# Kernel optimization log

Hardware: AMD Instinct MI355X
Metric: run time of the kernel (lower is better)

Reference implementation:

```python
import jax, jax.numpy as jnp
import numpy as np

B, C, IMG, P = 8, 6, 384, 16
DIM, HEADS, DEPTH, MLP, NCLS = 768, 12, 4, 3072, 1000
N = (IMG // P) ** 2            # 576 patches
DH = DIM // HEADS              # 64
PATCH_DIM = C * P * P          # 1536


def setup_inputs() -> dict:
    key = jax.random.key(0)
    ks = jax.random.split(key, 13)
    f = lambda k, shp, s=0.02: jax.random.normal(k, shp, jnp.float32) * s
    return {
        "x": jax.random.normal(ks[0], (B, C, IMG, IMG), jnp.float32),
        "patch_w": f(ks[1], (PATCH_DIM, DIM)),
        "patch_b": f(ks[2], (DIM,)),
        "ln1_g": jnp.ones((DEPTH, DIM), jnp.float32),
        "ln1_b": jnp.zeros((DEPTH, DIM), jnp.float32),
        "w_qkv": f(ks[3], (DEPTH, DIM, 3 * DIM)),
        "bias_att": f(ks[4], (DEPTH, HEADS, N, N), 0.5),
        "w_out": f(ks[5], (DEPTH, DIM, DIM)),
        "ln2_g": jnp.ones((DEPTH, DIM), jnp.float32),
        "ln2_b": jnp.zeros((DEPTH, DIM), jnp.float32),
        "w1": f(ks[6], (DEPTH, DIM, MLP)),
        "b1": f(ks[7], (DEPTH, MLP)),
        "w2": f(ks[8], (DEPTH, MLP, DIM)),
        "b2": f(ks[9], (DEPTH, DIM)),
        "lnh_g": jnp.ones((DIM,), jnp.float32),
        "lnh_b": jnp.zeros((DIM,), jnp.float32),
        "w_head": f(ks[10], (DIM, NCLS)),
        "b_head": f(ks[11], (NCLS,)),
    }


def _ln(x, g, b, eps=1e-5):
    m = x.mean(-1, keepdims=True)
    v = ((x - m) ** 2).mean(-1, keepdims=True)
    return (x - m) * jax.lax.rsqrt(v + eps) * g + b


def _patchify(x, patch_w, patch_b):
    # Rearrange 'b c (h p1) (w p2) -> b (h w) (p1 p2 c)' then Linear(patch_dim, dim)
    b = x.shape[0]
    g = IMG // P
    x = x.reshape(b, C, g, P, g, P).transpose(0, 2, 4, 3, 5, 1).reshape(b, g * g, PATCH_DIM)
    return x @ patch_w + patch_b


def _forward(x, patch_w, patch_b, ln1_g, ln1_b, w_qkv, bias_att, w_out,
             ln2_g, ln2_b, w1, b1, w2, b2, lnh_g, lnh_b, w_head, b_head):
    scale = DH ** -0.5
    tok = _patchify(x, patch_w, patch_b)  # [B, N, DIM]; pos_info='mul_att_normed' -> no pos_embed added

    def block(t, p):
        l1g, l1b, wqkv, bias, wout, l2g, l2b, ww1, bb1, ww2, bb2 = p
        h = _ln(t, l1g, l1b)
        qkv = h @ wqkv                                     # [B, N, 3*DIM]
        q, k, v = jnp.split(qkv, 3, axis=-1)
        rs = lambda a: a.reshape(t.shape[0], N, HEADS, DH).transpose(0, 2, 1, 3)
        q, k, v = rs(q), rs(k), rs(v)                      # [B, H, N, DH]
        dots = jnp.einsum('bhid,bhjd->bhij', q, k) * scale
        # mul_att_normed: softmax(qk) * softmax(bias), renormalized over keys
        attn = jax.nn.softmax(dots, axis=-1) * jax.nn.softmax(bias, axis=-1)[None]
        attn = attn / attn.sum(-1, keepdims=True)
        o = jnp.einsum('bhij,bhjd->bhid', attn, v)
        o = o.transpose(0, 2, 1, 3).reshape(t.shape[0], N, DIM) @ wout
        t = t + o
        h2 = _ln(t, l2g, l2b)
        t = t + (jax.nn.gelu(h2 @ ww1 + bb1, approximate=False) @ ww2 + bb2)
        return t, None

    tok, _ = jax.lax.scan(block, tok,
                          (ln1_g, ln1_b, w_qkv, bias_att, w_out,
                           ln2_g, ln2_b, w1, b1, w2, b2))
    pooled = tok.mean(axis=1)                              # mean-pool tokens
    return _ln(pooled, lnh_g, lnh_b) @ w_head + b_head     # [B, NCLS]


def reference(x, patch_w, patch_b, ln1_g, ln1_b, w_qkv, bias_att, w_out,
              ln2_g, ln2_b, w1, b1, w2, b2, lnh_g, lnh_b, w_head, b_head):
    return _forward(x, patch_w, patch_b, ln1_g, ln1_b, w_qkv, bias_att, w_out,
                    ln2_g, ln2_b, w1, b1, w2, b2, lnh_g, lnh_b, w_head, b_head)
```

## Files before the change

### kernel.cpp

```cpp
#include <hip/hip_runtime.h>
#include <hip/hip_bf16.h>

typedef __attribute__((ext_vector_type(8))) short bf16x8;
typedef __attribute__((ext_vector_type(4))) float f32x4;

#define DEVI __device__ __forceinline__

DEVI unsigned short f2bf_bits(float f) {
    __hip_bfloat16 h = __float2bfloat16(f);
    return *reinterpret_cast<unsigned short*>(&h);
}

DEVI void gload_lds16(const void* g, void* lds) {
    __builtin_amdgcn_global_load_lds(
        (const __attribute__((address_space(1))) unsigned int*)g,
        (__attribute__((address_space(3))) unsigned int*)lds, 16, 0, 0);
}

template <int N> DEVI void wait_vm() {
    if constexpr (N == 0) asm volatile("s_waitcnt vmcnt(0)" ::: "memory");
    else if constexpr (N == 3) asm volatile("s_waitcnt vmcnt(3)" ::: "memory");
    else if constexpr (N == 6) asm volatile("s_waitcnt vmcnt(6)" ::: "memory");
    else if constexpr (N == 12) asm volatile("s_waitcnt vmcnt(12)" ::: "memory");
    __builtin_amdgcn_sched_barrier(0);
}

DEVI int2 remap2d(int bid, int total, int gx) {
    int q = total >> 3, r = total & 7, x = bid & 7, l = bid >> 3;
    int seq = (x < r ? x * (q + 1) : r * (q + 1) + (x - r) * q) + l;
    int g4 = seq / (4 * gx);
    int rem = seq - g4 * 4 * gx;
    return {g4 * 4 + (rem & 3), rem >> 2};
}

__global__ __launch_bounds__(256) void patchify_kernel(const float* __restrict__ x,
                                                       unsigned short* __restrict__ patches)
{
    size_t t8 = (size_t)blockIdx.x * 256 + threadIdx.x;
    int jq = (int)(t8 % 48);
    size_t t = t8 / 48;
    int r = (int)(t % 384); t /= 384;
    int c = (int)(t % 6);
    int b = (int)(t / 6);
    int j = jq * 8;
    int gh = r >> 4, p1 = r & 15, gw = j >> 4, p2 = j & 15;
    int prow = b * 576 + gh * 24 + gw;
    int pcol = c * 256 + p1 * 16 + p2;
    const float* src = x + ((((size_t)b * 6 + c) * 384 + r) * 384 + j);
    float4 v0 = ((const float4*)src)[0];
    float4 v1 = ((const float4*)src)[1];
    ushort u[8] = { f2bf_bits(v0.x), f2bf_bits(v0.y), f2bf_bits(v0.z), f2bf_bits(v0.w),
                    f2bf_bits(v1.x), f2bf_bits(v1.y), f2bf_bits(v1.z), f2bf_bits(v1.w) };
    *(int4*)&patches[(size_t)prow * 1536 + pcol] = *(int4*)u;
}

__global__ __launch_bounds__(256) void convT_patch_kernel(const float* __restrict__ W,
                                                          __hip_bfloat16* __restrict__ Wt)
{
    __shared__ float tile[32][33];
    int n0 = blockIdx.x * 32, kp0 = blockIdx.y * 32;
    int tx = threadIdx.x & 31, ty = threadIdx.x >> 5;
#pragma unroll
    for (int i = 0; i < 4; i++) {
        int kp = kp0 + ty + 8 * i;
        int k = (kp & 255) * 6 + (kp >> 8);
        tile[ty + 8 * i][tx] = W[(size_t)k * 768 + n0 + tx];
    }
    __syncthreads();
#pragma unroll
    for (int i = 0; i < 4; i++)
        Wt[(size_t)(n0 + ty + 8 * i) * 1536 + kp0 + tx] = __float2bfloat16(tile[tx][ty + 8 * i]);
}

DEVI void convT_body(const float* __restrict__ W, __hip_bfloat16* __restrict__ Wt,
                     int K, int N, int k0, int n0, int tid)
{
    __shared__ float tile[32][33];
    int tx = tid & 31, ty = tid >> 5;
#pragma unroll
    for (int i = 0; i < 4; i++)
        tile[ty + 8 * i][tx] = W[(size_t)(k0 + ty + 8 * i) * N + n0 + tx];
    __syncthreads();
#pragma unroll
    for (int i = 0; i < 4; i++)
        Wt[(size_t)(n0 + ty + 8 * i) * K + k0 + tx] = __float2bfloat16(tile[tx][ty + 8 * i]);
}

__global__ __launch_bounds__(256) void convT4_kernel(const float* __restrict__ wqkv,
                                                     const float* __restrict__ wout,
                                                     const float* __restrict__ w1,
                                                     const float* __restrict__ w2,
                                                     __hip_bfloat16* __restrict__ dst)
{
    int bt = blockIdx.x;
    const float* W; __hip_bfloat16* Wt; int K, N, lt;
    if (bt < 1728)      { W = wqkv; K = 768;  N = 2304; lt = bt;        Wt = dst; }
    else if (bt < 2304) { W = wout; K = 768;  N = 768;  lt = bt - 1728; Wt = dst + 1769472; }
    else if (bt < 4608) { W = w1;   K = 768;  N = 3072; lt = bt - 2304; Wt = dst + 2359296; }
    else                { W = w2;   K = 3072; N = 768;  lt = bt - 4608; Wt = dst + 4718592; }
    int tn = N >> 5;
    convT_body(W, Wt, K, N, (lt / tn) * 32, (lt % tn) * 32, threadIdx.x);
}

DEVI void st_ln(float* p, float v) { *p = v; }
DEVI void st_ln(__hip_bfloat16* p, float v) { *p = __float2bfloat16(v); }

template <typename OutT>
__global__ __launch_bounds__(256) void ln_kernel(const float* __restrict__ x,
                                                 const float* __restrict__ g,
                                                 const float* __restrict__ b,
                                                 OutT* __restrict__ out)
{
    int row = blockIdx.x, tid = threadIdx.x;
    const float* xr = x + (size_t)row * 768;
    float v0 = xr[tid], v1 = xr[tid + 256], v2 = xr[tid + 512];
    float s = v0 + v1 + v2;
    float s2 = v0 * v0 + v1 * v1 + v2 * v2;
#pragma unroll
    for (int m = 32; m >= 1; m >>= 1) { s += __shfl_xor(s, m); s2 += __shfl_xor(s2, m); }
    __shared__ float red[8];
    int w = tid >> 6;
    if ((tid & 63) == 0) { red[w] = s; red[4 + w] = s2; }
    __syncthreads();
    s = red[0] + red[1] + red[2] + red[3];
    s2 = red[4] + red[5] + red[6] + red[7];
    float mean = s * (1.0f / 768.0f);
    float var = s2 * (1.0f / 768.0f) - mean * mean;
    float rstd = rsqrtf(var + 1e-5f);
    OutT* orow = out + (size_t)row * 768;
    st_ln(&orow[tid], (v0 - mean) * rstd * g[tid] + b[tid]);
    st_ln(&orow[tid + 256], (v1 - mean) * rstd * g[tid + 256] + b[tid + 256]);
    st_ln(&orow[tid + 512], (v2 - mean) * rstd * g[tid + 512] + b[tid + 512]);
}

template <bool BIAS, bool RESID, bool GELU>
__global__ __launch_bounds__(256, 3) void gemm_bt_kernel(
    const __hip_bfloat16* __restrict__ A,
    const __hip_bfloat16* __restrict__ Bt,
    const float* __restrict__ bias,
    const float* __restrict__ resid,
    float* __restrict__ Cf,
    int M, int N, int K, int gx)
{
    constexpr int BM = 64, SL = 3;
    __shared__ __align__(16) __hip_bfloat16 As[3][BM * 32];
    __shared__ __align__(16) __hip_bfloat16 Bs[3][128 * 32];
    const int tid = threadIdx.x;
    const int wid = tid >> 6, lane = tid & 63;
    const int g = lane >> 4, l16 = lane & 15;
    const int wm = (wid >> 1) * 32, wn = (wid & 1) * 64;

    int2 bc = remap2d(blockIdx.x, gridDim.x, gx);
    const int bm = bc.x * BM, bn = bc.y * 128;

    const int sr = tid >> 2;
    const int csrc = (lane & 3) ^ ((lane >> 3) & 3);
    const int sdst = sr * 32 + (lane & 3) * 8;
    size_t aOff = (size_t)(bm + sr) * K + csrc * 8;
    size_t bOff[2];
#pragma unroll
    for (int i = 0; i < 2; i++) bOff[i] = (size_t)(bn + i * 64 + sr) * K + csrc * 8;

    auto stage = [&](__hip_bfloat16* asb, __hip_bfloat16* bsb, int tq) {
        const __hip_bfloat16* ap = A + tq * 32;
        const __hip_bfloat16* bp = Bt + tq * 32;
        gload_lds16(ap + aOff, asb + sdst);
#pragma unroll
        for (int i = 0; i < 2; i++) gload_lds16(bp + bOff[i], bsb + i * 2048 + sdst);
    };

    const int pSw = (l16 >> 1) & 3;
    f32x4 acc[2][4] = {};
    const int nt = K >> 5;

    stage(As[0], Bs[0], 0);
    stage(As[1], Bs[1], 1);
    stage(As[2], Bs[2], 2);
    wait_vm<2 * SL>();
    __builtin_amdgcn_s_barrier();
    __builtin_amdgcn_sched_barrier(0);

    for (int t = 0; t < nt; t += 3) {
#pragma unroll
        for (int u = 0; u < 3; u++) {
            const int tc = t + u;
            bf16x8 af[2], bfr[4];
#pragma unroll
            for (int mi = 0; mi < 2; mi++)
                af[mi] = *(const bf16x8*)&As[u][(wm + mi * 16 + l16) * 32 + ((g ^ pSw) << 3)];
#pragma unroll
            for (int ni = 0; ni < 4; ni++)
                bfr[ni] = *(const bf16x8*)&Bs[u][(wn + ni * 16 + l16) * 32 + ((g ^ pSw) << 3)];
            __builtin_amdgcn_s_setprio(1);
#pragma unroll
            for (int mi = 0; mi < 2; mi++)
#pragma unroll
                for (int ni = 0; ni < 4; ni++)
                    acc[mi][ni] = __builtin_amdgcn_mfma_f32_16x16x32_bf16(af[mi], bfr[ni], acc[mi][ni], 0, 0, 0);
            __builtin_amdgcn_s_setprio(0);

            asm volatile("s_waitcnt lgkmcnt(0)" ::: "memory");
            __builtin_amdgcn_sched_barrier(0);
            __builtin_amdgcn_s_barrier();
            __builtin_amdgcn_sched_barrier(0);

            if (tc + 3 < nt) stage(As[u], Bs[u], tc + 3);
            if (tc + 1 < nt) {
                if (tc + 4 <= nt)      wait_vm<2 * SL>();
                else if (tc + 3 == nt) wait_vm<SL>();
                else                   wait_vm<0>();
                __builtin_amdgcn_s_barrier();
                __builtin_amdgcn_sched_barrier(0);
            }
        }
    }

#pragma unroll
    for (int mi = 0; mi < 2; mi++) {
#pragma unroll
        for (int ni = 0; ni < 4; ni++) {
            int gcol = bn + wn + ni * 16 + l16;
            float bval = 0.0f;
            if (BIAS) bval = bias[gcol];
#pragma unroll
            for (int r = 0; r < 4; r++) {
                int grow = bm + wm + mi * 16 + 4 * g + r;
                float v = acc[mi][ni][r] + bval;
                if (GELU) v = 0.5f * v * (1.0f + erff(v * 0.70710678118654752f));
                if (RESID) v += resid[(size_t)grow * N + gcol];
                Cf[(size_t)grow * N + gcol] = v;
            }
        }
    }
}

template <bool BIAS, bool GELU>
__global__ __launch_bounds__(256, 2) void gemm_wide_kernel(
    const __hip_bfloat16* __restrict__ A,
    const __hip_bfloat16* __restrict__ Bt,
    const float* __restrict__ bias,
    __hip_bfloat16* __restrict__ Cb,
    int M, int N, int K, int gx)
{
    constexpr int SL = 6;
    __shared__ __align__(16) __hip_bfloat16 As[3][128 * 32];
    __shared__ __align__(16) __hip_bfloat16 Bs[3][256 * 32];
    const int tid = threadIdx.x;
    const int wid = tid >> 6, lane = tid & 63;
    const int g = lane >> 4, l16 = lane & 15;
    const int wm = (wid >> 1) * 64, wn = (wid & 1) * 128;

    int2 bc = remap2d(blockIdx.x, gridDim.x, gx);
    const int bm = bc.x * 128, bn = bc.y * 256;

    const int sr = tid >> 2;
    const int csrc = (lane & 3) ^ ((lane >> 3) & 3);
    const int sdst = sr * 32 + (lane & 3) * 8;
    size_t aOff[2], bOff[4];
#pragma unroll
    for (int i = 0; i < 2; i++) aOff[i] = (size_t)(bm + i * 64 + sr) * K + csrc * 8;
#pragma unroll
    for (int i = 0; i < 4; i++) bOff[i] = (size_t)(bn + i * 64 + sr) * K + csrc * 8;

    auto stage = [&](__hip_bfloat16* asb, __hip_bfloat16* bsb, int tq) {
        const __hip_bfloat16* ap = A + tq * 32;
        const __hip_bfloat16* bp = Bt + tq * 32;
#pragma unroll
        for (int i = 0; i < 2; i++) gload_lds16(ap + aOff[i], asb + i * 2048 + sdst);
#pragma unroll
        for (int i = 0; i < 4; i++) gload_lds16(bp + bOff[i], bsb + i * 2048 + sdst);
    };

    const int pSw = (l16 >> 1) & 3;
    f32x4 acc[4][8] = {};
    const int nt = K >> 5;

    stage(As[0], Bs[0], 0);
    stage(As[1], Bs[1], 1);
    stage(As[2], Bs[2], 2);
    wait_vm<2 * SL>();
    __builtin_amdgcn_s_barrier();
    __builtin_amdgcn_sched_barrier(0);

    for (int t = 0; t < nt; t += 3) {
#pragma unroll
        for (int u = 0; u < 3; u++) {
            const int tc = t + u;
            bf16x8 af[4], bfr[8];
#pragma unroll
            for (int mi = 0; mi < 4; mi++)
                af[mi] = *(const bf16x8*)&As[u][(wm + mi * 16 + l16) * 32 + ((g ^ pSw) << 3)];
#pragma unroll
            for (int ni = 0; ni < 8; ni++)
                bfr[ni] = *(const bf16x8*)&Bs[u][(wn + ni * 16 + l16) * 32 + ((g ^ pSw) << 3)];
            __builtin_amdgcn_s_setprio(1);
#pragma unroll
            for (int mi = 0; mi < 4; mi++)
#pragma unroll
                for (int ni = 0; ni < 8; ni++)
                    acc[mi][ni] = __builtin_amdgcn_mfma_f32_16x16x32_bf16(af[mi], bfr[ni], acc[mi][ni], 0, 0, 0);
            __builtin_amdgcn_s_setprio(0);

            asm volatile("s_waitcnt lgkmcnt(0)" ::: "memory");
            __builtin_amdgcn_sched_barrier(0);
            __builtin_amdgcn_s_barrier();
            __builtin_amdgcn_sched_barrier(0);

            if (tc + 3 < nt) stage(As[u], Bs[u], tc + 3);
            if (tc + 1 < nt) {
                if (tc + 4 <= nt)      wait_vm<2 * SL>();
                else if (tc + 3 == nt) wait_vm<SL>();
                else                   wait_vm<0>();
                __builtin_amdgcn_s_barrier();
                __builtin_amdgcn_sched_barrier(0);
            }
        }
    }

    __hip_bfloat16* scr = &As[0][0] + wid * (16 * 136);
#pragma unroll
    for (int mi = 0; mi < 4; mi++) {
#pragma unroll
        for (int ni = 0; ni < 8; ni++) {
            int gcol = bn + wn + ni * 16 + l16;
            float bval = 0.0f;
            if (BIAS) bval = bias[gcol];
#pragma unroll
            for (int r = 0; r < 4; r++) {
                float v = acc[mi][ni][r] + bval;
                if (GELU) v = 0.5f * v * (1.0f + erff(v * 0.70710678118654752f));
                scr[(4 * g + r) * 136 + ni * 16 + l16] = __float2bfloat16(v);
            }
        }
        asm volatile("s_waitcnt lgkmcnt(0)" ::: "memory");
        __builtin_amdgcn_sched_barrier(0);
#pragma unroll
        for (int q2 = 0; q2 < 4; q2++) {
            int idx = q2 * 64 + lane;
            int row16 = idx >> 4, ch = idx & 15;
            bf16x8 vv = *(const bf16x8*)&scr[row16 * 136 + ch * 8];
            int grow = bm + wm + mi * 16 + row16;
            *(int4*)&Cb[(size_t)grow * N + bn + wn + ch * 8] = *(int4*)&vv;
        }
        asm volatile("s_waitcnt lgkmcnt(0)" ::: "memory");
        __builtin_amdgcn_sched_barrier(0);
    }
}

__global__ __launch_bounds__(256) void attn_kernel(const __hip_bfloat16* __restrict__ qkvb,
                                                   const float* __restrict__ bias,
                                                   unsigned short* __restrict__ o)
{
    const int seq = (blockIdx.x & 7) * 108 + (blockIdx.x >> 3);
    const int bb = seq & 7, qt = (seq >> 3) % 9, h = seq / 72;
    const int q0 = qt * 64;
    const int tid = threadIdx.x;
    const int wq = tid >> 6, lane = tid & 63, g = lane >> 4, l16 = lane & 15;

    __shared__ __align__(16) unsigned short Qs[64 * 72];
    __shared__ __align__(16) unsigned short Ks[64 * 72];
    __shared__ __align__(16) unsigned short Vt[64 * 72];
    __shared__ __align__(16) unsigned short Ps[4][16 * 72];

    {
        int r = tid >> 2, cb = (tid & 3) * 16;
        const int4* s4 = (const int4*)&qkvb[(size_t)(bb * 576 + q0 + r) * 2304 + h * 64 + cb];
        int4* d4 = (int4*)&Qs[r * 72 + cb];
        d4[0] = s4[0]; d4[1] = s4[1];
    }
    __syncthreads();
    bf16x8 qf0 = *(const bf16x8*)&Qs[(wq * 16 + l16) * 72 + g * 8];
    bf16x8 qf1 = *(const bf16x8*)&Qs[(wq * 16 + l16) * 72 + 32 + g * 8];

    float m_r[4] = {-1e30f, -1e30f, -1e30f, -1e30f};
    float l_r[4] = {0.f, 0.f, 0.f, 0.f};
    f32x4 oa[4] = {};
    const float* bias_h = bias + (size_t)h * 576 * 576;
    const float scale = 0.125f;

    for (int kt = 0; kt < 576; kt += 64) {
        {
            int r = tid >> 2, cb = (tid & 3) * 16;
            const int4* s4 = (const int4*)&qkvb[(size_t)(bb * 576 + kt + r) * 2304 + 768 + h * 64 + cb];
            int4* d4 = (int4*)&Ks[r * 72 + cb];
            d4[0] = s4[0]; d4[1] = s4[1];
            int key = tid & 63, d0 = (tid >> 6) * 16;
            const unsigned short* vs = (const unsigned short*)&qkvb[(size_t)(bb * 576 + kt + key) * 2304 + 1536 + h * 64 + d0];
            bf16x8 v0 = *(const bf16x8*)vs;
            bf16x8 v1 = *(const bf16x8*)(vs + 8);
#pragma unroll
            for (int e = 0; e < 8; e++) {
                Vt[(d0 + e) * 72 + key] = (unsigned short)v0[e];
                Vt[(d0 + 8 + e) * 72 + key] = (unsigned short)v1[e];
            }
        }
        __syncthreads();

        float bl[4][4];
#pragma unroll
        for (int kc = 0; kc < 4; kc++)
#pragma unroll
            for (int r = 0; r < 4; r++) {
                int q = q0 + wq * 16 + 4 * g + r;
                bl[kc][r] = bias_h[(size_t)q * 576 + kt + kc * 16 + l16];
            }

        f32x4 sc[4] = {};
        __builtin_amdgcn_s_setprio(1);
#pragma unroll
        for (int kc = 0; kc < 4; kc++) {
            bf16x8 kf0 = *(const bf16x8*)&Ks[(kc * 16 + l16) * 72 + g * 8];
            bf16x8 kf1 = *(const bf16x8*)&Ks[(kc * 16 + l16) * 72 + 32 + g * 8];
            sc[kc] = __builtin_amdgcn_mfma_f32_16x16x32_bf16(qf0, kf0, sc[kc], 0, 0, 0);
            sc[kc] = __builtin_amdgcn_mfma_f32_16x16x32_bf16(qf1, kf1, sc[kc], 0, 0, 0);
        }
        __builtin_amdgcn_s_setprio(0);

        float sv[4][4], mt[4] = {-1e30f, -1e30f, -1e30f, -1e30f};
#pragma unroll
        for (int kc = 0; kc < 4; kc++)
#pragma unroll
            for (int r = 0; r < 4; r++) {
                float s = sc[kc][r] * scale + bl[kc][r];
                sv[kc][r] = s;
                mt[r] = fmaxf(mt[r], s);
            }
#pragma unroll
        for (int r = 0; r < 4; r++)
#pragma unroll
            for (int m = 1; m < 16; m <<= 1) mt[r] = fmaxf(mt[r], __shfl_xor(mt[r], m));

        float sf[4];
#pragma unroll
        for (int r = 0; r < 4; r++) {
            float mn = fmaxf(m_r[r], mt[r]);
            sf[r] = __expf(m_r[r] - mn);
            m_r[r] = mn;
        }
        float rs[4] = {0.f, 0.f, 0.f, 0.f};
#pragma unroll
        for (int kc = 0; kc < 4; kc++)
#pragma unroll
            for (int r = 0; r < 4; r++) {
                float p = __expf(sv[kc][r] - m_r[r]);
                rs[r] += p;
                Ps[wq][(4 * g + r) * 72 + kc * 16 + l16] = f2bf_bits(p);
            }
#pragma unroll
        for (int r = 0; r < 4; r++) {
#pragma unroll
            for (int m = 1; m < 16; m <<= 1) rs[r] += __shfl_xor(rs[r], m);
            l_r[r] = l_r[r] * sf[r] + rs[r];
        }
#pragma unroll
        for (int dt = 0; dt < 4; dt++)
#pragma unroll
            for (int r = 0; r < 4; r++) oa[dt][r] *= sf[r];

        asm volatile("s_waitcnt lgkmcnt(0)" ::: "memory");

        __builtin_amdgcn_s_setprio(1);
#pragma unroll
        for (int s = 0; s < 2; s++) {
            bf16x8 pf = *(const bf16x8*)&Ps[wq][l16 * 72 + s * 32 + g * 8];
#pragma unroll
            for (int dt = 0; dt < 4; dt++) {
                bf16x8 vf = *(const bf16x8*)&Vt[(dt * 16 + l16) * 72 + s * 32 + g * 8];
                oa[dt] = __builtin_amdgcn_mfma_f32_16x16x32_bf16(pf, vf, oa[dt], 0, 0, 0);
            }
        }
        __builtin_amdgcn_s_setprio(0);
        __syncthreads();
    }

#pragma unroll
    for (int dt = 0; dt < 4; dt++)
#pragma unroll
        for (int r = 0; r < 4; r++) {
            int q = q0 + wq * 16 + 4 * g + r;
            float v = oa[dt][r] / l_r[r];
            o[(size_t)(bb * 576 + q) * 768 + h * 64 + dt * 16 + l16] = f2bf_bits(v);
        }
}

__global__ __launch_bounds__(256) void pool_kernel(const float* __restrict__ tok, float* __restrict__ pooled)
{
    int d = blockIdx.x * 256 + threadIdx.x;
    int b = blockIdx.y;
    float s = 0.0f;
    for (int n = 0; n < 576; n++) s += tok[(size_t)(b * 576 + n) * 768 + d];
    pooled[b * 768 + d] = s * (1.0f / 576.0f);
}

__global__ __launch_bounds__(256) void head_kernel(const float* __restrict__ lnp,
                                                   const float* __restrict__ w,
                                                   const float* __restrict__ bh,
                                                   float* __restrict__ out)
{
    int c = blockIdx.x * 256 + threadIdx.x;
    int b = blockIdx.y;
    if (c >= 1000) return;
    float s = bh[c];
    for (int d = 0; d < 768; d++) s += lnp[b * 768 + d] * w[(size_t)d * 1000 + c];
    out[b * 1000 + c] = s;
}

extern "C" void kernel_launch(void* const* d_in, const int* in_sizes, int n_in,
                              void* d_out, int out_size, void* d_ws, size_t ws_size,
                              hipStream_t stream)
{
    const float* x = (const float*)d_in[0];
    const float* patch_w = (const float*)d_in[1];
    const float* patch_b = (const float*)d_in[2];
    const float* ln1_g = (const float*)d_in[3];
    const float* ln1_b = (const float*)d_in[4];
    const float* w_qkv = (const float*)d_in[5];
    const float* bias_att = (const float*)d_in[6];
    const float* w_out = (const float*)d_in[7];
    const float* ln2_g = (const float*)d_in[8];
    const float* ln2_b = (const float*)d_in[9];
    const float* w1 = (const float*)d_in[10];
    const float* b1 = (const float*)d_in[11];
    const float* w2 = (const float*)d_in[12];
    const float* b2 = (const float*)d_in[13];
    const float* lnh_g = (const float*)d_in[14];
    const float* lnh_b = (const float*)d_in[15];
    const float* w_head = (const float*)d_in[16];
    const float* b_head = (const float*)d_in[17];
    float* out = (float*)d_out;

    char* ws = (char*)d_ws;
    float* tok = (float*)(ws + 0);
    __hip_bfloat16* qkv_bf = (__hip_bfloat16*)(ws + 14155776);
    float* pooled = (float*)(ws + 56623104);
    float* pooledln = (float*)(ws + 56647680);
    __hip_bfloat16* patches = (__hip_bfloat16*)(ws + 56672256);
    __hip_bfloat16* lw = patches;
    __hip_bfloat16* h_bf = (__hip_bfloat16*)(ws + 70828032);
    __hip_bfloat16* o_bf = (__hip_bfloat16*)(ws + 77905920);
    __hip_bfloat16* hid_bf = (__hip_bfloat16*)(ws + 84983808);
    __hip_bfloat16* wbuf = (__hip_bfloat16*)(ws + 113295360);

    patchify_kernel<<<3456, 256, 0, stream>>>(x, (unsigned short*)patches);
    convT_patch_kernel<<<dim3(24, 48), 256, 0, stream>>>(patch_w, wbuf);
    gemm_bt_kernel<true, false, false><<<432, 256, 0, stream>>>(
        patches, wbuf, patch_b, nullptr, tok, 4608, 768, 1536, 6);

    for (int l = 0; l < 4; l++) {
        convT4_kernel<<<6912, 256, 0, stream>>>(
            w_qkv + (size_t)l * 768 * 2304, w_out + (size_t)l * 768 * 768,
            w1 + (size_t)l * 768 * 3072, w2 + (size_t)l * 3072 * 768, lw);
        ln_kernel<__hip_bfloat16><<<4608, 256, 0, stream>>>(tok, ln1_g + l * 768, ln1_b + l * 768, h_bf);
        gemm_wide_kernel<false, false><<<324, 256, 0, stream>>>(
            h_bf, lw, nullptr, qkv_bf, 4608, 2304, 768, 9);
        attn_kernel<<<864, 256, 0, stream>>>(
            qkv_bf, bias_att + (size_t)l * 12 * 576 * 576, (unsigned short*)o_bf);
        gemm_bt_kernel<false, true, false><<<432, 256, 0, stream>>>(
            o_bf, lw + 1769472, nullptr, tok, tok, 4608, 768, 768, 6);
        ln_kernel<__hip_bfloat16><<<4608, 256, 0, stream>>>(tok, ln2_g + l * 768, ln2_b + l * 768, h_bf);
        gemm_wide_kernel<true, true><<<432, 256, 0, stream>>>(
            h_bf, lw + 2359296, b1 + l * 3072, hid_bf, 4608, 3072, 768, 12);
        gemm_bt_kernel<true, true, false><<<432, 256, 0, stream>>>(
            hid_bf, lw + 4718592, b2 + l * 768, tok, tok, 4608, 768, 3072, 6);
    }

    pool_kernel<<<dim3(3, 8), 256, 0, stream>>>(tok, pooled);
    ln_kernel<float><<<8, 256, 0, stream>>>(pooled, lnh_g, lnh_b, pooledln);
    head_kernel<<<dim3(4, 8), 256, 0, stream>>>(pooledln, w_head, b_head, out);
}
```

Measured before the change: 910.3 us.

## Store residual stream in bf16 with LDS-staged vectorized GEMM epilogue

Switches the token/residual buffer from fp32 to bf16, so the LayerNorm, pooling and residual-add GEMMs read and write half the bytes. The narrow GEMM epilogue now stages each warp's tile through shared memory and writes 16-byte vectors, with the residual also loaded as vectors. Block scheduling changes to a simple column-major remap, and the MFMA priority hints are removed. The residual accumulation now rounds to bf16 at every layer, which loses precision.

```diff
diff --git a/kernel.cpp b/kernel.cpp
--- a/kernel.cpp
+++ b/kernel.cpp
@@ -9,6 +9,10 @@
 DEVI unsigned short f2bf_bits(float f) {
     __hip_bfloat16 h = __float2bfloat16(f);
     return *reinterpret_cast<unsigned short*>(&h);
+}
+DEVI float bfbits2f(unsigned short u) {
+    __hip_bfloat16 h = *reinterpret_cast<__hip_bfloat16*>(&u);
+    return __bfloat162float(h);
 }
 
 DEVI void gload_lds16(const void* g, void* lds) {
@@ -25,12 +29,10 @@
     __builtin_amdgcn_sched_barrier(0);
 }
 
-DEVI int2 remap2d(int bid, int total, int gx) {
+DEVI int2 remap_cm(int bid, int total, int nrow) {
     int q = total >> 3, r = total & 7, x = bid & 7, l = bid >> 3;
     int seq = (x < r ? x * (q + 1) : r * (q + 1) + (x - r) * q) + l;
-    int g4 = seq / (4 * gx);
-    int rem = seq - g4 * 4 * gx;
-    return {g4 * 4 + (rem & 3), rem >> 2};
+    return {seq % nrow, seq / nrow};
 }
 
 __global__ __launch_bounds__(256) void patchify_kernel(const float* __restrict__ x,
@@ -102,18 +104,20 @@
     convT_body(W, Wt, K, N, (lt / tn) * 32, (lt % tn) * 32, threadIdx.x);
 }
 
+DEVI float ld_ln(const float* p) { return *p; }
+DEVI float ld_ln(const __hip_bfloat16* p) { return __bfloat162float(*p); }
 DEVI void st_ln(float* p, float v) { *p = v; }
 DEVI void st_ln(__hip_bfloat16* p, float v) { *p = __float2bfloat16(v); }
 
-template <typename OutT>
-__global__ __launch_bounds__(256) void ln_kernel(const float* __restrict__ x,
+template <typename InT, typename OutT>
+__global__ __launch_bounds__(256) void ln_kernel(const InT* __restrict__ x,
                                                  const float* __restrict__ g,
                                                  const float* __restrict__ b,
                                                  OutT* __restrict__ out)
 {
     int row = blockIdx.x, tid = threadIdx.x;
-    const float* xr = x + (size_t)row * 768;
-    float v0 = xr[tid], v1 = xr[tid + 256], v2 = xr[tid + 512];
+    const InT* xr = x + (size_t)row * 768;
+    float v0 = ld_ln(&xr[tid]), v1 = ld_ln(&xr[tid + 256]), v2 = ld_ln(&xr[tid + 512]);
     float s = v0 + v1 + v2;
     float s2 = v0 * v0 + v1 * v1 + v2 * v2;
 #pragma unroll
@@ -133,14 +137,14 @@
     st_ln(&orow[tid + 512], (v2 - mean) * rstd * g[tid + 512] + b[tid + 512]);
 }
 
-template <bool BIAS, bool RESID, bool GELU>
+template <bool BIAS, bool RESID>
 __global__ __launch_bounds__(256, 3) void gemm_bt_kernel(
     const __hip_bfloat16* __restrict__ A,
     const __hip_bfloat16* __restrict__ Bt,
     const float* __restrict__ bias,
-    const float* __restrict__ resid,
-    float* __restrict__ Cf,
-    int M, int N, int K, int gx)
+    const __hip_bfloat16* __restrict__ resid,
+    __hip_bfloat16* __restrict__ Cb,
+    int M, int N, int K, int nrow)
 {
     constexpr int BM = 64, SL = 3;
     __shared__ __align__(16) __hip_bfloat16 As[3][BM * 32];
@@ -150,7 +154,7 @@
     const int g = lane >> 4, l16 = lane & 15;
     const int wm = (wid >> 1) * 32, wn = (wid & 1) * 64;
 
-    int2 bc = remap2d(blockIdx.x, gridDim.x, gx);
+    int2 bc = remap_cm(blockIdx.x, gridDim.x, nrow);
     const int bm = bc.x * BM, bn = bc.y * 128;
 
     const int sr = tid >> 2;
@@ -191,13 +195,11 @@
 #pragma unroll
             for (int ni = 0; ni < 4; ni++)
                 bfr[ni] = *(const bf16x8*)&Bs[u][(wn + ni * 16 + l16) * 32 + ((g ^ pSw) << 3)];
-            __builtin_amdgcn_s_setprio(1);
 #pragma unroll
             for (int mi = 0; mi < 2; mi++)
 #pragma unroll
                 for (int ni = 0; ni < 4; ni++)
                     acc[mi][ni] = __builtin_amdgcn_mfma_f32_16x16x32_bf16(af[mi], bfr[ni], acc[mi][ni], 0, 0, 0);
-            __builtin_amdgcn_s_setprio(0);
 
             asm volatile("s_waitcnt lgkmcnt(0)" ::: "memory");
             __builtin_amdgcn_sched_barrier(0);
@@ -215,22 +217,35 @@
         }
     }
 
+    __hip_bfloat16* scr = &As[0][0] + wid * (16 * 72);
 #pragma unroll
     for (int mi = 0; mi < 2; mi++) {
 #pragma unroll
         for (int ni = 0; ni < 4; ni++) {
-            int gcol = bn + wn + ni * 16 + l16;
             float bval = 0.0f;
-            if (BIAS) bval = bias[gcol];
-#pragma unroll
-            for (int r = 0; r < 4; r++) {
-                int grow = bm + wm + mi * 16 + 4 * g + r;
-                float v = acc[mi][ni][r] + bval;
-                if (GELU) v = 0.5f * v * (1.0f + erff(v * 0.70710678118654752f));
-                if (RESID) v += resid[(size_t)grow * N + gcol];
-                Cf[(size_t)grow * N + gcol] = v;
-            }
-        }
+            if (BIAS) bval = bias[bn + wn + ni * 16 + l16];
+#pragma unroll
+            for (int r = 0; r < 4; r++)
+                scr[(4 * g + r) * 72 + ni * 16 + l16] = __float2bfloat16(acc[mi][ni][r] + bval);
+        }
+        asm volatile("s_waitcnt lgkmcnt(0)" ::: "memory");
+        __builtin_amdgcn_sched_barrier(0);
+#pragma unroll
+        for (int q2 = 0; q2 < 2; q2++) {
+            int row16 = q2 * 8 + (lane >> 3), ch = lane & 7;
+            bf16x8 vv = *(const bf16x8*)&scr[row16 * 72 + ch * 8];
+            int grow = bm + wm + mi * 16 + row16;
+            size_t off = (size_t)grow * N + bn + wn + ch * 8;
+            if (RESID) {
+                bf16x8 rv = *(const bf16x8*)&resid[off];
+#pragma unroll
+                for (int e = 0; e < 8; e++)
+                    vv[e] = (short)f2bf_bits(bfbits2f((unsigned short)vv[e]) + bfbits2f((unsigned short)rv[e]));
+            }
+            *(int4*)&Cb[off] = *(int4*)&vv;
+        }
+        asm volatile("s_waitcnt lgkmcnt(0)" ::: "memory");
+        __builtin_amdgcn_sched_barrier(0);
     }
 }
 
@@ -240,7 +255,7 @@
     const __hip_bfloat16* __restrict__ Bt,
     const float* __restrict__ bias,
     __hip_bfloat16* __restrict__ Cb,
-    int M, int N, int K, int gx)
+    int M, int N, int K, int nrow)
 {
     constexpr int SL = 6;
     __shared__ __align__(16) __hip_bfloat16 As[3][128 * 32];
@@ -250,7 +265,7 @@
     const int g = lane >> 4, l16 = lane & 15;
     const int wm = (wid >> 1) * 64, wn = (wid & 1) * 128;
 
-    int2 bc = remap2d(blockIdx.x, gridDim.x, gx);
+    int2 bc = remap_cm(blockIdx.x, gridDim.x, nrow);
     const int bm = bc.x * 128, bn = bc.y * 256;
 
     const int sr = tid >> 2;
@@ -293,13 +308,11 @@
 #pragma unroll
             for (int ni = 0; ni < 8; ni++)
                 bfr[ni] = *(const bf16x8*)&Bs[u][(wn + ni * 16 + l16) * 32 + ((g ^ pSw) << 3)];
-            __builtin_amdgcn_s_setprio(1);
 #pragma unroll
             for (int mi = 0; mi < 4; mi++)
 #pragma unroll
                 for (int ni = 0; ni < 8; ni++)
                     acc[mi][ni] = __builtin_amdgcn_mfma_f32_16x16x32_bf16(af[mi], bfr[ni], acc[mi][ni], 0, 0, 0);
-            __builtin_amdgcn_s_setprio(0);
 
             asm volatile("s_waitcnt lgkmcnt(0)" ::: "memory");
             __builtin_amdgcn_sched_barrier(0);
@@ -322,9 +335,8 @@
     for (int mi = 0; mi < 4; mi++) {
 #pragma unroll
         for (int ni = 0; ni < 8; ni++) {
-            int gcol = bn + wn + ni * 16 + l16;
             float bval = 0.0f;
-            if (BIAS) bval = bias[gcol];
+            if (BIAS) bval = bias[bn + wn + ni * 16 + l16];
 #pragma unroll
             for (int r = 0; r < 4; r++) {
                 float v = acc[mi][ni][r] + bval;
@@ -483,12 +495,13 @@
         }
 }
 
-__global__ __launch_bounds__(256) void pool_kernel(const float* __restrict__ tok, float* __restrict__ pooled)
+__global__ __launch_bounds__(256) void pool_kernel(const __hip_bfloat16* __restrict__ tok,
+                                                   float* __restrict__ pooled)
 {
     int d = blockIdx.x * 256 + threadIdx.x;
     int b = blockIdx.y;
     float s = 0.0f;
-    for (int n = 0; n < 576; n++) s += tok[(size_t)(b * 576 + n) * 768 + d];
+    for (int n = 0; n < 576; n++) s += __bfloat162float(tok[(size_t)(b * 576 + n) * 768 + d]);
     pooled[b * 768 + d] = s * (1.0f / 576.0f);
 }
 
@@ -530,7 +543,7 @@
     float* out = (float*)d_out;
 
     char* ws = (char*)d_ws;
-    float* tok = (float*)(ws + 0);
+    __hip_bfloat16* tok = (__hip_bfloat16*)(ws + 0);
     __hip_bfloat16* qkv_bf = (__hip_bfloat16*)(ws + 14155776);
     float* pooled = (float*)(ws + 56623104);
     float* pooledln = (float*)(ws + 56647680);
@@ -543,28 +556,30 @@
 
     patchify_kernel<<<3456, 256, 0, stream>>>(x, (unsigned short*)patches);
     convT_patch_kernel<<<dim3(24, 48), 256, 0, stream>>>(patch_w, wbuf);
-    gemm_bt_kernel<true, false, false><<<432, 256, 0, stream>>>(
-        patches, wbuf, patch_b, nullptr, tok, 4608, 768, 1536, 6);
+    gemm_bt_kernel<true, false><<<432, 256, 0, stream>>>(
+        patches, wbuf, patch_b, nullptr, tok, 4608, 768, 1536, 72);
 
     for (int l = 0; l < 4; l++) {
         convT4_kernel<<<6912, 256, 0, stream>>>(
             w_qkv + (size_t)l * 768 * 2304, w_out + (size_t)l * 768 * 768,
             w1 + (size_t)l * 768 * 3072, w2 + (size_t)l * 3072 * 768, lw);
-        ln_kernel<__hip_bfloat16><<<4608, 256, 0, stream>>>(tok, ln1_g + l * 768, ln1_b + l * 768, h_bf);
+        ln_kernel<__hip_bfloat16, __hip_bfloat16><<<4608, 256, 0, stream>>>(
+            tok, ln1_g + l * 768, ln1_b + l * 768, h_bf);
         gemm_wide_kernel<false, false><<<324, 256, 0, stream>>>(
-            h_bf, lw, nullptr, qkv_bf, 4608, 2304, 768, 9);
+            h_bf, lw, nullptr, qkv_bf, 4608, 2304, 768, 36);
         attn_kernel<<<864, 256, 0, stream>>>(
             qkv_bf, bias_att + (size_t)l * 12 * 576 * 576, (unsigned short*)o_bf);
-        gemm_bt_kernel<false, true, false><<<432, 256, 0, stream>>>(
-            o_bf, lw + 1769472, nullptr, tok, tok, 4608, 768, 768, 6);
-        ln_kernel<__hip_bfloat16><<<4608, 256, 0, stream>>>(tok, ln2_g + l * 768, ln2_b + l * 768, h_bf);
+        gemm_bt_kernel<false, true><<<432, 256, 0, stream>>>(
+            o_bf, lw + 1769472, nullptr, tok, tok, 4608, 768, 768, 72);
+        ln_kernel<__hip_bfloat16, __hip_bfloat16><<<4608, 256, 0, stream>>>(
+            tok, ln2_g + l * 768, ln2_b + l * 768, h_bf);
         gemm_wide_kernel<true, true><<<432, 256, 0, stream>>>(
-            h_bf, lw + 2359296, b1 + l * 3072, hid_bf, 4608, 3072, 768, 12);
-        gemm_bt_kernel<true, true, false><<<432, 256, 0, stream>>>(
-            hid_bf, lw + 4718592, b2 + l * 768, tok, tok, 4608, 768, 3072, 6);
+            h_bf, lw + 2359296, b1 + l * 3072, hid_bf, 4608, 3072, 768, 36);
+        gemm_bt_kernel<true, true><<<432, 256, 0, stream>>>(
+            hid_bf, lw + 4718592, b2 + l * 768, tok, tok, 4608, 768, 3072, 72);
     }
 
     pool_kernel<<<dim3(3, 8), 256, 0, stream>>>(tok, pooled);
-    ln_kernel<float><<<8, 256, 0, stream>>>(pooled, lnh_g, lnh_b, pooledln);
+    ln_kernel<float, float><<<8, 256, 0, stream>>>(pooled, lnh_g, lnh_b, pooledln);
     head_kernel<<<dim3(4, 8), 256, 0, stream>>>(pooledln, w_head, b_head, out);
 }
```

Result: no change. 922.2 us (+1.3%).
